# Performance work log

Measured on AMD Instinct MI355X. Metric: run time of the kernel, lower is better.

Reference implementation:

```python
import jax, jax.numpy as jnp
import numpy as np

TOP_K = 2


def setup_inputs() -> dict:
    key = jax.random.key(0)
    k0, k1, k2, k3, k4 = jax.random.split(key, 5)
    B, S, H, F, E = 2, 1024, 2048, 7168, 8
    scale = 0.02
    return {
        "hidden_states": jax.random.normal(k0, (B, S, H), jnp.float32),
        "Wg": jax.random.normal(k1, (E, H), jnp.float32) * scale,
        "w1": jax.random.normal(k2, (E, F, H), jnp.float32) * scale,
        "w3": jax.random.normal(k3, (E, F, H), jnp.float32) * scale,
        "w2": jax.random.normal(k4, (E, H, F), jnp.float32) * scale,
    }


def reference(hidden_states, Wg, w1, w3, w2):
    B, S, H = hidden_states.shape
    E = Wg.shape[0]
    x = hidden_states.reshape(-1, H)                      # [T, H]
    T = x.shape[0]

    # Router: logits -> softmax (float32) -> top-k -> renormalize
    router_logits = jnp.einsum("th,eh->te", x, Wg)        # [T, E]
    probs = jax.nn.softmax(router_logits.astype(jnp.float32), axis=-1)
    top_w, top_idx = jax.lax.top_k(probs, TOP_K)          # [T, K]
    top_w = top_w / jnp.sum(top_w, axis=-1, keepdims=True)
    top_w = top_w.astype(x.dtype)

    # Combine weights: [T, E], zero for unselected experts
    combine = jnp.zeros((T, E), x.dtype).at[
        jnp.arange(T)[:, None], top_idx
    ].add(top_w)

    out = jnp.zeros((T, H), x.dtype)
    for e in range(E):
        h = jax.nn.silu(x @ w1[e].T) * (x @ w3[e].T)      # [T, F]
        out = out + (h @ w2[e].T) * combine[:, e:e + 1]   # [T, H]

    return out.reshape(B, S, H), router_logits
```

## Files before the change

kernel.cpp:

```cpp
#include <hip/hip_runtime.h>

#define T_TOK 2048
#define H_DIM 2048
#define F_DIM 7168
#define E_NUM 8
#define MAX_SLOTS 5120
#define N13 (2 * F_DIM)

typedef __attribute__((ext_vector_type(8))) _Float16 f16x8;
typedef __attribute__((ext_vector_type(4))) float    f32x4;

#define GLL(g, l) __builtin_amdgcn_global_load_lds(                          \
    (const __attribute__((address_space(1))) void*)(g),                      \
    (__attribute__((address_space(3))) void*)(l), 16, 0, 0)


__global__ __launch_bounds__(256) void cvt13_kernel(const float* __restrict__ w1,
                                                    const float* __restrict__ w3,
                                                    _Float16* __restrict__ w13h) {
    int b = blockIdx.x;
    int e = b / N13;
    int c = b - e * N13;
    int blk = c >> 6, sub = c & 63;
    int f = blk * 32 + (sub & 31);
    const float* src = (sub < 32 ? w1 : w3) + ((size_t)e * F_DIM + f) * H_DIM + threadIdx.x * 8;
    _Float16* dst = w13h + (size_t)b * H_DIM + threadIdx.x * 8;
    float4 a = *(const float4*)src;
    float4 bb = *(const float4*)(src + 4);
    f16x8 h;
    h[0]=(_Float16)a.x;  h[1]=(_Float16)a.y;  h[2]=(_Float16)a.z;  h[3]=(_Float16)a.w;
    h[4]=(_Float16)bb.x; h[5]=(_Float16)bb.y; h[6]=(_Float16)bb.z; h[7]=(_Float16)bb.w;
    *(f16x8*)dst = h;
}

__global__ __launch_bounds__(256) void cvtw_kernel(const float* __restrict__ src,
                                                   _Float16* __restrict__ dst) {
    size_t i = ((size_t)blockIdx.x * 256 + threadIdx.x) * 8;
    float4 a = *(const float4*)(src + i);
    float4 b = *(const float4*)(src + i + 4);
    f16x8 h;
    h[0]=(_Float16)a.x; h[1]=(_Float16)a.y; h[2]=(_Float16)a.z; h[3]=(_Float16)a.w;
    h[4]=(_Float16)b.x; h[5]=(_Float16)b.y; h[6]=(_Float16)b.z; h[7]=(_Float16)b.w;
    *(f16x8*)(dst + i) = h;
}


__global__ __launch_bounds__(256) void router_kernel(
    const float* __restrict__ x, const float* __restrict__ wg,
    float* __restrict__ logits_out, int* __restrict__ tk_e,
    float* __restrict__ tk_w, int* __restrict__ meta) {
    int wave = threadIdx.x >> 6;
    int lane = threadIdx.x & 63;
    int t = blockIdx.x * 4 + wave;
    const float* xr = x + (size_t)t * H_DIM;

    float xv[32];
#pragma unroll
    for (int i = 0; i < 8; i++) {
        float4 v = *(const float4*)(xr + i * 256 + lane * 4);
        xv[i*4+0] = v.x; xv[i*4+1] = v.y; xv[i*4+2] = v.z; xv[i*4+3] = v.w;
    }
    float lg[E_NUM];
#pragma unroll
    for (int e = 0; e < E_NUM; e++) {
        const float* wr = wg + (size_t)e * H_DIM;
        float acc = 0.f;
#pragma unroll
        for (int i = 0; i < 8; i++) {
            float4 v = *(const float4*)(wr + i * 256 + lane * 4);
            acc += xv[i*4+0]*v.x + xv[i*4+1]*v.y + xv[i*4+2]*v.z + xv[i*4+3]*v.w;
        }
#pragma unroll
        for (int s = 32; s > 0; s >>= 1) acc += __shfl_xor(acc, s, 64);
        lg[e] = acc;
    }
    if (lane == 0) {
        float b0 = -3e38f, b1 = -3e38f; int i0 = 0, i1 = 0;
#pragma unroll
        for (int e = 0; e < E_NUM; e++) {
            float le = lg[e];
            if (le > b0)      { b1 = b0; i1 = i0; b0 = le; i0 = e; }
            else if (le > b1) { b1 = le; i1 = e; }
        }
        float w0 = 1.f / (1.f + __expf(b1 - b0));
        float w1v = 1.f - w0;
#pragma unroll
        for (int e = 0; e < E_NUM; e++) logits_out[(size_t)t * E_NUM + e] = lg[e];
        tk_e[t*2+0] = i0; tk_w[t*2+0] = w0;
        tk_e[t*2+1] = i1; tk_w[t*2+1] = w1v;
        atomicAdd(&meta[i0], 1);
        atomicAdd(&meta[i1], 1);
    }
}

__global__ void scan_kernel(int* __restrict__ meta, int* __restrict__ slot_tok,
                            float* __restrict__ slot_w) {
    int lane = threadIdx.x;
    int cnts[E_NUM], pads[E_NUM], bases[E_NUM];
    int run = 0;
#pragma unroll
    for (int e = 0; e < E_NUM; e++) {
        cnts[e] = meta[e];
        pads[e] = (cnts[e] + 127) & ~127;
        bases[e] = run;
        run += pads[e];
    }
    if (lane < E_NUM) { meta[8 + lane] = pads[lane]; meta[16 + lane] = bases[lane]; }
    for (int e = 0; e < E_NUM; e++)
        for (int i = cnts[e] + lane; i < pads[e]; i += 64) {
            slot_tok[bases[e] + i] = 0;
            slot_w[bases[e] + i] = 0.f;
        }
}

__global__ __launch_bounds__(256) void assign_kernel(
    const int* __restrict__ tk_e, const float* __restrict__ tk_w,
    int* __restrict__ meta, int* __restrict__ slot_tok, float* __restrict__ slot_w) {
    int t = blockIdx.x * 256 + threadIdx.x;
    if (t >= T_TOK) return;
#pragma unroll
    for (int k = 0; k < 2; k++) {
        int e = tk_e[t*2+k];
        int pos = atomicAdd(&meta[24 + e], 1);
        int s = meta[16 + e] + pos;
        slot_tok[s] = t;
        slot_w[s] = tk_w[t*2+k];
    }
}

__global__ __launch_bounds__(512, 2) void ffn1_kernel(
    const _Float16* __restrict__ xb, const _Float16* __restrict__ w13h,
    const int* __restrict__ slot_tok, const int* __restrict__ meta,
    _Float16* __restrict__ hbuf) {
    int e = blockIdx.z;
    int cntpad = meta[8 + e];
    int mb = blockIdx.y;
    if (mb * 256 >= cntpad) return;
    int base = meta[16 + e];
    int nb = blockIdx.x;

    __shared__ _Float16 sA[2][256][64];
    __shared__ _Float16 sB[2][256][64];

    int tid  = threadIdx.x;
    int lane = tid & 63;
    int wave = tid >> 6;
    int wm = wave >> 2, wn = wave & 3;
    int w8 = wave * 8;

    int lr = lane & 15;
    int sw = lane & 7;
    int sg = lane >> 4;
    int offk0 = lr * 64 + ((sg    ) ^ sw) * 8;
    int offk1 = lr * 64 + ((sg + 4) ^ sw) * 8;

    int rsub = lane >> 3;
    int sl   = (lane & 7) ^ rsub;
    int slot0 = base + mb * 256;

    const _Float16* aG[4];
    const _Float16* bG[4];
#pragma unroll
    for (int q = 0; q < 4; q++) {
        int r = mb * 256 + q * 64 + w8 + rsub;
        int tok = (r < cntpad) ? slot_tok[base + r] : 0;
        aG[q] = xb + (size_t)tok * H_DIM + sl * 8;
        bG[q] = w13h + ((size_t)e * N13 + (size_t)nb * 256 + q * 64 + w8 + rsub) * H_DIM + sl * 8;
    }

    f32x4 zero = {0.f, 0.f, 0.f, 0.f};
    f32x4 acc[8][4];
#pragma unroll
    for (int m = 0; m < 8; m++)
#pragma unroll
        for (int n = 0; n < 4; n++) acc[m][n] = zero;

    const int NT = H_DIM / 64;
#pragma unroll
    for (int q = 0; q < 4; q++) GLL(aG[q] + 0,  &sA[0][q*64 + w8][0]);
#pragma unroll
    for (int q = 0; q < 4; q++) GLL(bG[q] + 0,  &sB[0][q*64 + w8][0]);
#pragma unroll
    for (int q = 0; q < 4; q++) GLL(aG[q] + 64, &sA[1][q*64 + w8][0]);
#pragma unroll
    for (int q = 0; q < 4; q++) GLL(bG[q] + 64, &sB[1][q*64 + w8][0]);

    for (int t = 0; t < NT; ++t) {
        if (t < NT - 1) asm volatile("s_waitcnt vmcnt(8)" ::: "memory");
        else            asm volatile("s_waitcnt vmcnt(0)" ::: "memory");
        __builtin_amdgcn_sched_barrier(0);
        __builtin_amdgcn_s_barrier();
        __builtin_amdgcn_sched_barrier(0);
        int bd = t & 1;
        const _Float16* Ab = &sA[bd][wm * 128][0];
        const _Float16* Bb = &sB[bd][wn * 64][0];
        f16x8 bf[2][4];
#pragma unroll
        for (int n = 0; n < 4; n++) {
            bf[0][n] = *(const f16x8*)(const void*)(Bb + n * 1024 + offk0);
            bf[1][n] = *(const f16x8*)(const void*)(Bb + n * 1024 + offk1);
        }
        __builtin_amdgcn_s_setprio(1);
#pragma unroll
        for (int m = 0; m < 8; m++) {
            f16x8 a0 = *(const f16x8*)(const void*)(Ab + m * 1024 + offk0);
            f16x8 a1 = *(const f16x8*)(const void*)(Ab + m * 1024 + offk1);
#pragma unroll
            for (int n = 0; n < 4; n++) {
                acc[m][n] = __builtin_amdgcn_mfma_f32_16x16x32_f16(a0, bf[0][n], acc[m][n], 0, 0, 0);
                acc[m][n] = __builtin_amdgcn_mfma_f32_16x16x32_f16(a1, bf[1][n], acc[m][n], 0, 0, 0);
            }
        }
        __builtin_amdgcn_s_setprio(0);
        __builtin_amdgcn_sched_barrier(0);
        __builtin_amdgcn_s_barrier();
        __builtin_amdgcn_sched_barrier(0);
        if (t + 2 < NT) {
            int k2 = (t + 2) * 64;
#pragma unroll
            for (int q = 0; q < 4; q++) GLL(aG[q] + k2, &sA[bd][q*64 + w8][0]);
#pragma unroll
            for (int q = 0; q < 4; q++) GLL(bG[q] + k2, &sB[bd][q*64 + w8][0]);
        }
    }

    int row_e0 = mb * 256 + wm * 128;
    int fb = nb * 128 + wn * 32;
#pragma unroll
    for (int m = 0; m < 8; m++) {
#pragma unroll
        for (int j = 0; j < 4; j++) {
            int re = row_e0 + m * 16 + (lane >> 4) * 4 + j;
            if (re < cntpad) {
                size_t srow = (size_t)(base + re) * F_DIM;
#pragma unroll
                for (int n = 0; n < 2; n++) {
                    float a1 = acc[m][n][j], a3 = acc[m][n + 2][j];
                    float hv = a1 * a3 / (1.f + __expf(-a1));
                    hbuf[srow + fb + n * 16 + lr] = (_Float16)hv;
                }
            }
        }
    }
}

__global__ __launch_bounds__(512, 2) void ffn2_kernel(
    const _Float16* __restrict__ hbuf, const _Float16* __restrict__ w2h,
    const int* __restrict__ slot_tok, const float* __restrict__ slot_w,
    const int* __restrict__ meta, float* __restrict__ out) {
    int e = blockIdx.z;
    int cntpad = meta[8 + e];
    int mb = blockIdx.y;
    if (mb * 128 >= cntpad) return;
    int base = meta[16 + e];
    int nb = blockIdx.x;

    __shared__ _Float16 sA[2][128][64];
    __shared__ _Float16 sB[2][256][64];

    int tid  = threadIdx.x;
    int lane = tid & 63;
    int wave = tid >> 6;
    int wm = wave >> 2, wn = wave & 3;
    int w8 = wave * 8;

    int lr = lane & 15;
    int sw = lane & 7;
    int sg = lane >> 4;
    int offk0 = lr * 64 + ((sg    ) ^ sw) * 8;
    int offk1 = lr * 64 + ((sg + 4) ^ sw) * 8;

    int rsub = lane >> 3;
    int sl   = (lane & 7) ^ rsub;
    int slot0 = base + mb * 128;

    const _Float16* aG[2];
    const _Float16* bG[4];
#pragma unroll
    for (int q = 0; q < 2; q++)
        aG[q] = hbuf + (size_t)(slot0 + q * 64 + w8 + rsub) * F_DIM + sl * 8;
#pragma unroll
    for (int q = 0; q < 4; q++)
        bG[q] = w2h + ((size_t)e * H_DIM + (size_t)nb * 256 + q * 64 + w8 + rsub) * F_DIM + sl * 8;

    f32x4 zero = {0.f, 0.f, 0.f, 0.f};
    f32x4 acc[4][4];
#pragma unroll
    for (int m = 0; m < 4; m++)
#pragma unroll
        for (int n = 0; n < 4; n++) acc[m][n] = zero;

    const int NT = F_DIM / 64;
#pragma unroll
    for (int q = 0; q < 2; q++) GLL(aG[q] + 0,  &sA[0][q*64 + w8][0]);
#pragma unroll
    for (int q = 0; q < 4; q++) GLL(bG[q] + 0,  &sB[0][q*64 + w8][0]);
#pragma unroll
    for (int q = 0; q < 2; q++) GLL(aG[q] + 64, &sA[1][q*64 + w8][0]);
#pragma unroll
    for (int q = 0; q < 4; q++) GLL(bG[q] + 64, &sB[1][q*64 + w8][0]);

    for (int t = 0; t < NT; ++t) {
        if (t < NT - 1) asm volatile("s_waitcnt vmcnt(6)" ::: "memory");
        else            asm volatile("s_waitcnt vmcnt(0)" ::: "memory");
        __builtin_amdgcn_sched_barrier(0);
        __builtin_amdgcn_s_barrier();
        __builtin_amdgcn_sched_barrier(0);
        int bd = t & 1;
        const _Float16* Ab = &sA[bd][wm * 64][0];
        const _Float16* Bb = &sB[bd][wn * 64][0];
        f16x8 bf[2][4];
#pragma unroll
        for (int n = 0; n < 4; n++) {
            bf[0][n] = *(const f16x8*)(const void*)(Bb + n * 1024 + offk0);
            bf[1][n] = *(const f16x8*)(const void*)(Bb + n * 1024 + offk1);
        }
        __builtin_amdgcn_s_setprio(1);
#pragma unroll
        for (int m = 0; m < 4; m++) {
            f16x8 a0 = *(const f16x8*)(const void*)(Ab + m * 1024 + offk0);
            f16x8 a1 = *(const f16x8*)(const void*)(Ab + m * 1024 + offk1);
#pragma unroll
            for (int n = 0; n < 4; n++) {
                acc[m][n] = __builtin_amdgcn_mfma_f32_16x16x32_f16(a0, bf[0][n], acc[m][n], 0, 0, 0);
                acc[m][n] = __builtin_amdgcn_mfma_f32_16x16x32_f16(a1, bf[1][n], acc[m][n], 0, 0, 0);
            }
        }
        __builtin_amdgcn_s_setprio(0);
        __builtin_amdgcn_sched_barrier(0);
        __builtin_amdgcn_s_barrier();
        __builtin_amdgcn_sched_barrier(0);
        if (t + 2 < NT) {
            int k2 = (t + 2) * 64;
#pragma unroll
            for (int q = 0; q < 2; q++) GLL(aG[q] + k2, &sA[bd][q*64 + w8][0]);
#pragma unroll
            for (int q = 0; q < 4; q++) GLL(bG[q] + k2, &sB[bd][q*64 + w8][0]);
        }
    }

    int row0 = mb * 128 + wm * 64;
    int col0 = nb * 256 + wn * 64;
#pragma unroll
    for (int m = 0; m < 4; m++) {
        int rb = row0 + m * 16 + (lane >> 4) * 4;
        int toks[4]; float wts[4];
#pragma unroll
        for (int j = 0; j < 4; j++) {
            int s = base + rb + j;
            toks[j] = slot_tok[s];
            wts[j]  = slot_w[s];
        }
#pragma unroll
        for (int n = 0; n < 4; n++) {
            int col = col0 + n * 16 + lr;
            f32x4 v = acc[m][n];
#pragma unroll
            for (int j = 0; j < 4; j++)
                atomicAdd(&out[(size_t)toks[j] * H_DIM + col], v[j] * wts[j]);
        }
    }
}

extern "C" void kernel_launch(void* const* d_in, const int* in_sizes, int n_in,
                              void* d_out, int out_size, void* d_ws, size_t ws_size,
                              hipStream_t stream) {
    const float* x  = (const float*)d_in[0];
    const float* wg = (const float*)d_in[1];
    const float* w1 = (const float*)d_in[2];
    const float* w3 = (const float*)d_in[3];
    const float* w2 = (const float*)d_in[4];
    float* out = (float*)d_out;
    float* logits = out + (size_t)T_TOK * H_DIM;

    const size_t WELEM = (size_t)E_NUM * F_DIM * H_DIM;

    char* ws = (char*)d_ws;
    _Float16* w13h = (_Float16*)ws;
    _Float16* w2h  = w13h + 2 * WELEM;
    _Float16* hbuf = w2h + WELEM;
    _Float16* xb   = hbuf + (size_t)MAX_SLOTS * F_DIM;
    char* p = (char*)(xb + (size_t)T_TOK * H_DIM);
    int*   slot_tok = (int*)p;   p += MAX_SLOTS * 4;
    float* slot_w   = (float*)p; p += MAX_SLOTS * 4;
    int*   tk_e     = (int*)p;   p += T_TOK * 2 * 4;
    float* tk_w     = (float*)p; p += T_TOK * 2 * 4;
    int*   meta     = (int*)p;

    hipMemsetAsync(d_out, 0, (size_t)out_size * sizeof(float), stream);
    hipMemsetAsync(meta, 0, 32 * sizeof(int), stream);

    cvt13_kernel<<<dim3(E_NUM * N13), 256, 0, stream>>>(w1, w3, w13h);
    cvtw_kernel<<<dim3(WELEM / (256 * 8)), 256, 0, stream>>>(w2, w2h);
    cvtw_kernel<<<dim3((size_t)T_TOK * H_DIM / (256 * 8)), 256, 0, stream>>>(x, xb);

    router_kernel<<<dim3(T_TOK / 4), 256, 0, stream>>>(x, wg, logits, tk_e, tk_w, meta);
    scan_kernel<<<dim3(1), 64, 0, stream>>>(meta, slot_tok, slot_w);
    assign_kernel<<<dim3(T_TOK / 256), 256, 0, stream>>>(tk_e, tk_w, meta, slot_tok, slot_w);

    ffn1_kernel<<<dim3(N13 / 256, 8, E_NUM), 512, 0, stream>>>(xb, w13h, slot_tok, meta, hbuf);
    ffn2_kernel<<<dim3(H_DIM / 256, 16, E_NUM), 512, 0, stream>>>(hbuf, w2h, slot_tok, slot_w, meta, out);
}
```

Baseline: 1.292 ms.

## Interleave A-chunk prefetch with MFMA and split-K FFN2 with 256-row tiles

Pads expert slots to 256 so row bounds checks can be dropped. The FFN1 and FFN2 main loops now split the A tile into four 64-row chunks and issue each chunk's global-to-LDS load between MFMA groups, using finer-grained barriers to overlap loads with compute. FFN2 moves to 256x256 tiles with a two-way split over the F dimension (grid z doubled), which relies on the existing atomicAdd output. The trade-off is more padding work, more atomics into the output, and more frequent barriers per K step.

```diff
diff --git a/kernel.cpp b/kernel.cpp
--- a/kernel.cpp
+++ b/kernel.cpp
@@ -4,7 +4,7 @@
 #define H_DIM 2048
 #define F_DIM 7168
 #define E_NUM 8
-#define MAX_SLOTS 5120
+#define MAX_SLOTS 6144
 #define N13 (2 * F_DIM)
 
 typedef __attribute__((ext_vector_type(8))) _Float16 f16x8;
@@ -101,7 +101,7 @@
 #pragma unroll
     for (int e = 0; e < E_NUM; e++) {
         cnts[e] = meta[e];
-        pads[e] = (cnts[e] + 127) & ~127;
+        pads[e] = (cnts[e] + 255) & ~255;
         bases[e] = run;
         run += pads[e];
     }
@@ -127,6 +127,7 @@
         slot_w[s] = tk_w[t*2+k];
     }
 }
+
 
 __global__ __launch_bounds__(512, 2) void ffn1_kernel(
     const _Float16* __restrict__ xb, const _Float16* __restrict__ w13h,
@@ -139,7 +140,7 @@
     int base = meta[16 + e];
     int nb = blockIdx.x;
 
-    __shared__ _Float16 sA[2][256][64];
+    __shared__ _Float16 sA[2][4][64][64];
     __shared__ _Float16 sB[2][256][64];
 
     int tid  = threadIdx.x;
@@ -147,26 +148,26 @@
     int wave = tid >> 6;
     int wm = wave >> 2, wn = wave & 3;
     int w8 = wave * 8;
-
-    int lr = lane & 15;
-    int sw = lane & 7;
-    int sg = lane >> 4;
-    int offk0 = lr * 64 + ((sg    ) ^ sw) * 8;
-    int offk1 = lr * 64 + ((sg + 4) ^ sw) * 8;
+    int lr  = lane & 15;
+    int sg  = lane >> 4;
+    int sw7 = lane & 7;
+    int so0 = ((sg    ) ^ sw7) * 8;
+    int so1 = ((sg + 4) ^ sw7) * 8;
 
     int rsub = lane >> 3;
-    int sl   = (lane & 7) ^ rsub;
-    int slot0 = base + mb * 256;
-
-    const _Float16* aG[4];
-    const _Float16* bG[4];
-#pragma unroll
-    for (int q = 0; q < 4; q++) {
-        int r = mb * 256 + q * 64 + w8 + rsub;
-        int tok = (r < cntpad) ? slot_tok[base + r] : 0;
-        aG[q] = xb + (size_t)tok * H_DIM + sl * 8;
-        bG[q] = w13h + ((size_t)e * N13 + (size_t)nb * 256 + q * 64 + w8 + rsub) * H_DIM + sl * 8;
-    }
+    int sl   = sw7 ^ rsub;
+    int s    = w8 + rsub;
+    const _Float16* aP[4];
+#pragma unroll
+    for (int c = 0; c < 4; c++) {
+        int trow = (s >> 5) * 128 + c * 32 + (s & 31);
+        int tok = slot_tok[base + mb * 256 + trow];
+        aP[c] = xb + (size_t)tok * H_DIM + sl * 8;
+    }
+    const _Float16* bP[4];
+#pragma unroll
+    for (int q = 0; q < 4; q++)
+        bP[q] = w13h + ((size_t)e * N13 + (size_t)nb * 256 + q * 64 + s) * H_DIM + sl * 8;
 
     f32x4 zero = {0.f, 0.f, 0.f, 0.f};
     f32x4 acc[8][4];
@@ -176,69 +177,86 @@
         for (int n = 0; n < 4; n++) acc[m][n] = zero;
 
     const int NT = H_DIM / 64;
-#pragma unroll
-    for (int q = 0; q < 4; q++) GLL(aG[q] + 0,  &sA[0][q*64 + w8][0]);
-#pragma unroll
-    for (int q = 0; q < 4; q++) GLL(bG[q] + 0,  &sB[0][q*64 + w8][0]);
-#pragma unroll
-    for (int q = 0; q < 4; q++) GLL(aG[q] + 64, &sA[1][q*64 + w8][0]);
-#pragma unroll
-    for (int q = 0; q < 4; q++) GLL(bG[q] + 64, &sB[1][q*64 + w8][0]);
+
+#pragma unroll
+    for (int c = 0; c < 4; c++) GLL(aP[c], &sA[0][c][w8][0]);
+#pragma unroll
+    for (int q = 0; q < 4; q++) GLL(bP[q], &sB[0][q * 64 + w8][0]);
+#pragma unroll
+    for (int c = 0; c < 3; c++) GLL(aP[c] + 64, &sA[1][c][w8][0]);
 
     for (int t = 0; t < NT; ++t) {
-        if (t < NT - 1) asm volatile("s_waitcnt vmcnt(8)" ::: "memory");
-        else            asm volatile("s_waitcnt vmcnt(0)" ::: "memory");
+        int cur = t & 1, nxt = cur ^ 1;
+        int kA1 = (t + 1) * 64, kA2 = (t + 2) * 64;
+
+        if (t + 1 < NT) {
+            GLL(aP[3] + kA1, &sA[nxt][3][w8][0]);
+            GLL(bP[0] + kA1, &sB[nxt][       w8][0]);
+            GLL(bP[1] + kA1, &sB[nxt][ 64 + w8][0]);
+            GLL(bP[2] + kA1, &sB[nxt][128 + w8][0]);
+            GLL(bP[3] + kA1, &sB[nxt][192 + w8][0]);
+            asm volatile("s_waitcnt vmcnt(8)" ::: "memory");
+        } else {
+            asm volatile("s_waitcnt vmcnt(0)" ::: "memory");
+        }
         __builtin_amdgcn_sched_barrier(0);
         __builtin_amdgcn_s_barrier();
-        __builtin_amdgcn_sched_barrier(0);
-        int bd = t & 1;
-        const _Float16* Ab = &sA[bd][wm * 128][0];
-        const _Float16* Bb = &sB[bd][wn * 64][0];
-        f16x8 bf[2][4];
+
+        f16x8 bf[4][2];
 #pragma unroll
         for (int n = 0; n < 4; n++) {
-            bf[0][n] = *(const f16x8*)(const void*)(Bb + n * 1024 + offk0);
-            bf[1][n] = *(const f16x8*)(const void*)(Bb + n * 1024 + offk1);
-        }
-        __builtin_amdgcn_s_setprio(1);
-#pragma unroll
-        for (int m = 0; m < 8; m++) {
-            f16x8 a0 = *(const f16x8*)(const void*)(Ab + m * 1024 + offk0);
-            f16x8 a1 = *(const f16x8*)(const void*)(Ab + m * 1024 + offk1);
+            bf[n][0] = *(const f16x8*)(const void*)&sB[cur][wn * 64 + n * 16 + lr][so0];
+            bf[n][1] = *(const f16x8*)(const void*)&sB[cur][wn * 64 + n * 16 + lr][so1];
+        }
+        {
+            f16x8 af0 = *(const f16x8*)(const void*)&sA[cur][0][wm * 32 + lr][so0];
+            f16x8 af1 = *(const f16x8*)(const void*)&sA[cur][0][wm * 32 + lr][so1];
+            f16x8 ag0 = *(const f16x8*)(const void*)&sA[cur][0][wm * 32 + 16 + lr][so0];
+            f16x8 ag1 = *(const f16x8*)(const void*)&sA[cur][0][wm * 32 + 16 + lr][so1];
+            __builtin_amdgcn_s_setprio(1);
 #pragma unroll
             for (int n = 0; n < 4; n++) {
-                acc[m][n] = __builtin_amdgcn_mfma_f32_16x16x32_f16(a0, bf[0][n], acc[m][n], 0, 0, 0);
-                acc[m][n] = __builtin_amdgcn_mfma_f32_16x16x32_f16(a1, bf[1][n], acc[m][n], 0, 0, 0);
+                acc[0][n] = __builtin_amdgcn_mfma_f32_16x16x32_f16(af0, bf[n][0], acc[0][n], 0, 0, 0);
+                acc[0][n] = __builtin_amdgcn_mfma_f32_16x16x32_f16(af1, bf[n][1], acc[0][n], 0, 0, 0);
+                acc[1][n] = __builtin_amdgcn_mfma_f32_16x16x32_f16(ag0, bf[n][0], acc[1][n], 0, 0, 0);
+                acc[1][n] = __builtin_amdgcn_mfma_f32_16x16x32_f16(ag1, bf[n][1], acc[1][n], 0, 0, 0);
             }
-        }
-        __builtin_amdgcn_s_setprio(0);
-        __builtin_amdgcn_sched_barrier(0);
+            __builtin_amdgcn_s_setprio(0);
+        }
         __builtin_amdgcn_s_barrier();
-        __builtin_amdgcn_sched_barrier(0);
-        if (t + 2 < NT) {
-            int k2 = (t + 2) * 64;
-#pragma unroll
-            for (int q = 0; q < 4; q++) GLL(aG[q] + k2, &sA[bd][q*64 + w8][0]);
-#pragma unroll
-            for (int q = 0; q < 4; q++) GLL(bG[q] + k2, &sB[bd][q*64 + w8][0]);
-        }
-    }
-
-    int row_e0 = mb * 256 + wm * 128;
-    int fb = nb * 128 + wn * 32;
+
+#pragma unroll
+        for (int q = 1; q < 4; ++q) {
+            if (t + 2 < NT) GLL(aP[q - 1] + kA2, &sA[cur][q - 1][w8][0]);
+            f16x8 af0 = *(const f16x8*)(const void*)&sA[cur][q][wm * 32 + lr][so0];
+            f16x8 af1 = *(const f16x8*)(const void*)&sA[cur][q][wm * 32 + lr][so1];
+            f16x8 ag0 = *(const f16x8*)(const void*)&sA[cur][q][wm * 32 + 16 + lr][so0];
+            f16x8 ag1 = *(const f16x8*)(const void*)&sA[cur][q][wm * 32 + 16 + lr][so1];
+            __builtin_amdgcn_s_setprio(1);
+#pragma unroll
+            for (int n = 0; n < 4; n++) {
+                acc[q*2+0][n] = __builtin_amdgcn_mfma_f32_16x16x32_f16(af0, bf[n][0], acc[q*2+0][n], 0, 0, 0);
+                acc[q*2+0][n] = __builtin_amdgcn_mfma_f32_16x16x32_f16(af1, bf[n][1], acc[q*2+0][n], 0, 0, 0);
+                acc[q*2+1][n] = __builtin_amdgcn_mfma_f32_16x16x32_f16(ag0, bf[n][0], acc[q*2+1][n], 0, 0, 0);
+                acc[q*2+1][n] = __builtin_amdgcn_mfma_f32_16x16x32_f16(ag1, bf[n][1], acc[q*2+1][n], 0, 0, 0);
+            }
+            __builtin_amdgcn_s_setprio(0);
+            __builtin_amdgcn_s_barrier();
+        }
+    }
+
+    int fb = (nb * 4 + wn) * 32;
 #pragma unroll
     for (int m = 0; m < 8; m++) {
 #pragma unroll
         for (int j = 0; j < 4; j++) {
-            int re = row_e0 + m * 16 + (lane >> 4) * 4 + j;
-            if (re < cntpad) {
-                size_t srow = (size_t)(base + re) * F_DIM;
-#pragma unroll
-                for (int n = 0; n < 2; n++) {
-                    float a1 = acc[m][n][j], a3 = acc[m][n + 2][j];
-                    float hv = a1 * a3 / (1.f + __expf(-a1));
-                    hbuf[srow + fb + n * 16 + lr] = (_Float16)hv;
-                }
+            int re = mb * 256 + wm * 128 + m * 16 + sg * 4 + j;
+            size_t srow = (size_t)(base + re) * F_DIM;
+#pragma unroll
+            for (int p = 0; p < 2; p++) {
+                float a1v = acc[m][p][j], a3v = acc[m][p + 2][j];
+                float hv = a1v * a3v / (1.f + __expf(-a1v));
+                hbuf[srow + fb + p * 16 + lr] = (_Float16)hv;
             }
         }
     }
@@ -248,14 +266,17 @@
     const _Float16* __restrict__ hbuf, const _Float16* __restrict__ w2h,
     const int* __restrict__ slot_tok, const float* __restrict__ slot_w,
     const int* __restrict__ meta, float* __restrict__ out) {
-    int e = blockIdx.z;
+    int ez = blockIdx.z;
+    int e = ez >> 1, ks = ez & 1;
     int cntpad = meta[8 + e];
     int mb = blockIdx.y;
-    if (mb * 128 >= cntpad) return;
+    if (mb * 256 >= cntpad) return;
     int base = meta[16 + e];
     int nb = blockIdx.x;
-
-    __shared__ _Float16 sA[2][128][64];
+    const int KOFF = ks * (F_DIM / 2);
+    const int NT = (F_DIM / 2) / 64;
+
+    __shared__ _Float16 sA[2][4][64][64];
     __shared__ _Float16 sB[2][256][64];
 
     int tid  = threadIdx.x;
@@ -263,93 +284,111 @@
     int wave = tid >> 6;
     int wm = wave >> 2, wn = wave & 3;
     int w8 = wave * 8;
-
-    int lr = lane & 15;
-    int sw = lane & 7;
-    int sg = lane >> 4;
-    int offk0 = lr * 64 + ((sg    ) ^ sw) * 8;
-    int offk1 = lr * 64 + ((sg + 4) ^ sw) * 8;
+    int lr  = lane & 15;
+    int sg  = lane >> 4;
+    int sw7 = lane & 7;
+    int so0 = ((sg    ) ^ sw7) * 8;
+    int so1 = ((sg + 4) ^ sw7) * 8;
 
     int rsub = lane >> 3;
-    int sl   = (lane & 7) ^ rsub;
-    int slot0 = base + mb * 128;
-
-    const _Float16* aG[2];
-    const _Float16* bG[4];
-#pragma unroll
-    for (int q = 0; q < 2; q++)
-        aG[q] = hbuf + (size_t)(slot0 + q * 64 + w8 + rsub) * F_DIM + sl * 8;
+    int sl   = sw7 ^ rsub;
+    int s    = w8 + rsub;
+    const _Float16* aP[4];
+#pragma unroll
+    for (int c = 0; c < 4; c++) {
+        int trow = (s >> 5) * 128 + c * 32 + (s & 31);
+        aP[c] = hbuf + (size_t)(base + mb * 256 + trow) * F_DIM + KOFF + sl * 8;
+    }
+    const _Float16* bP[4];
 #pragma unroll
     for (int q = 0; q < 4; q++)
-        bG[q] = w2h + ((size_t)e * H_DIM + (size_t)nb * 256 + q * 64 + w8 + rsub) * F_DIM + sl * 8;
+        bP[q] = w2h + ((size_t)e * H_DIM + (size_t)nb * 256 + q * 64 + s) * F_DIM + KOFF + sl * 8;
 
     f32x4 zero = {0.f, 0.f, 0.f, 0.f};
-    f32x4 acc[4][4];
-#pragma unroll
-    for (int m = 0; m < 4; m++)
+    f32x4 acc[8][4];
+#pragma unroll
+    for (int m = 0; m < 8; m++)
 #pragma unroll
         for (int n = 0; n < 4; n++) acc[m][n] = zero;
 
-    const int NT = F_DIM / 64;
-#pragma unroll
-    for (int q = 0; q < 2; q++) GLL(aG[q] + 0,  &sA[0][q*64 + w8][0]);
-#pragma unroll
-    for (int q = 0; q < 4; q++) GLL(bG[q] + 0,  &sB[0][q*64 + w8][0]);
-#pragma unroll
-    for (int q = 0; q < 2; q++) GLL(aG[q] + 64, &sA[1][q*64 + w8][0]);
-#pragma unroll
-    for (int q = 0; q < 4; q++) GLL(bG[q] + 64, &sB[1][q*64 + w8][0]);
+#pragma unroll
+    for (int c = 0; c < 4; c++) GLL(aP[c], &sA[0][c][w8][0]);
+#pragma unroll
+    for (int q = 0; q < 4; q++) GLL(bP[q], &sB[0][q * 64 + w8][0]);
+#pragma unroll
+    for (int c = 0; c < 3; c++) GLL(aP[c] + 64, &sA[1][c][w8][0]);
 
     for (int t = 0; t < NT; ++t) {
-        if (t < NT - 1) asm volatile("s_waitcnt vmcnt(6)" ::: "memory");
-        else            asm volatile("s_waitcnt vmcnt(0)" ::: "memory");
+        int cur = t & 1, nxt = cur ^ 1;
+        int kA1 = (t + 1) * 64, kA2 = (t + 2) * 64;
+
+        if (t + 1 < NT) {
+            GLL(aP[3] + kA1, &sA[nxt][3][w8][0]);
+            GLL(bP[0] + kA1, &sB[nxt][       w8][0]);
+            GLL(bP[1] + kA1, &sB[nxt][ 64 + w8][0]);
+            GLL(bP[2] + kA1, &sB[nxt][128 + w8][0]);
+            GLL(bP[3] + kA1, &sB[nxt][192 + w8][0]);
+            asm volatile("s_waitcnt vmcnt(8)" ::: "memory");
+        } else {
+            asm volatile("s_waitcnt vmcnt(0)" ::: "memory");
+        }
         __builtin_amdgcn_sched_barrier(0);
         __builtin_amdgcn_s_barrier();
-        __builtin_amdgcn_sched_barrier(0);
-        int bd = t & 1;
-        const _Float16* Ab = &sA[bd][wm * 64][0];
-        const _Float16* Bb = &sB[bd][wn * 64][0];
-        f16x8 bf[2][4];
+
+        f16x8 bf[4][2];
 #pragma unroll
         for (int n = 0; n < 4; n++) {
-            bf[0][n] = *(const f16x8*)(const void*)(Bb + n * 1024 + offk0);
-            bf[1][n] = *(const f16x8*)(const void*)(Bb + n * 1024 + offk1);
-        }
-        __builtin_amdgcn_s_setprio(1);
-#pragma unroll
-        for (int m = 0; m < 4; m++) {
-            f16x8 a0 = *(const f16x8*)(const void*)(Ab + m * 1024 + offk0);
-            f16x8 a1 = *(const f16x8*)(const void*)(Ab + m * 1024 + offk1);
+            bf[n][0] = *(const f16x8*)(const void*)&sB[cur][wn * 64 + n * 16 + lr][so0];
+            bf[n][1] = *(const f16x8*)(const void*)&sB[cur][wn * 64 + n * 16 + lr][so1];
+        }
+        {
+            f16x8 af0 = *(const f16x8*)(const void*)&sA[cur][0][wm * 32 + lr][so0];
+            f16x8 af1 = *(const f16x8*)(const void*)&sA[cur][0][wm * 32 + lr][so1];
+            f16x8 ag0 = *(const f16x8*)(const void*)&sA[cur][0][wm * 32 + 16 + lr][so0];
+            f16x8 ag1 = *(const f16x8*)(const void*)&sA[cur][0][wm * 32 + 16 + lr][so1];
+            __builtin_amdgcn_s_setprio(1);
 #pragma unroll
             for (int n = 0; n < 4; n++) {
-                acc[m][n] = __builtin_amdgcn_mfma_f32_16x16x32_f16(a0, bf[0][n], acc[m][n], 0, 0, 0);
-                acc[m][n] = __builtin_amdgcn_mfma_f32_16x16x32_f16(a1, bf[1][n], acc[m][n], 0, 0, 0);
+                acc[0][n] = __builtin_amdgcn_mfma_f32_16x16x32_f16(af0, bf[n][0], acc[0][n], 0, 0, 0);
+                acc[0][n] = __builtin_amdgcn_mfma_f32_16x16x32_f16(af1, bf[n][1], acc[0][n], 0, 0, 0);
+                acc[1][n] = __builtin_amdgcn_mfma_f32_16x16x32_f16(ag0, bf[n][0], acc[1][n], 0, 0, 0);
+                acc[1][n] = __builtin_amdgcn_mfma_f32_16x16x32_f16(ag1, bf[n][1], acc[1][n], 0, 0, 0);
             }
-        }
-        __builtin_amdgcn_s_setprio(0);
-        __builtin_amdgcn_sched_barrier(0);
+            __builtin_amdgcn_s_setprio(0);
+        }
         __builtin_amdgcn_s_barrier();
-        __builtin_amdgcn_sched_barrier(0);
-        if (t + 2 < NT) {
-            int k2 = (t + 2) * 64;
-#pragma unroll
-            for (int q = 0; q < 2; q++) GLL(aG[q] + k2, &sA[bd][q*64 + w8][0]);
-#pragma unroll
-            for (int q = 0; q < 4; q++) GLL(bG[q] + k2, &sB[bd][q*64 + w8][0]);
-        }
-    }
-
-    int row0 = mb * 128 + wm * 64;
+
+#pragma unroll
+        for (int q = 1; q < 4; ++q) {
+            if (t + 2 < NT) GLL(aP[q - 1] + kA2, &sA[cur][q - 1][w8][0]);
+            f16x8 af0 = *(const f16x8*)(const void*)&sA[cur][q][wm * 32 + lr][so0];
+            f16x8 af1 = *(const f16x8*)(const void*)&sA[cur][q][wm * 32 + lr][so1];
+            f16x8 ag0 = *(const f16x8*)(const void*)&sA[cur][q][wm * 32 + 16 + lr][so0];
+            f16x8 ag1 = *(const f16x8*)(const void*)&sA[cur][q][wm * 32 + 16 + lr][so1];
+            __builtin_amdgcn_s_setprio(1);
+#pragma unroll
+            for (int n = 0; n < 4; n++) {
+                acc[q*2+0][n] = __builtin_amdgcn_mfma_f32_16x16x32_f16(af0, bf[n][0], acc[q*2+0][n], 0, 0, 0);
+                acc[q*2+0][n] = __builtin_amdgcn_mfma_f32_16x16x32_f16(af1, bf[n][1], acc[q*2+0][n], 0, 0, 0);
+                acc[q*2+1][n] = __builtin_amdgcn_mfma_f32_16x16x32_f16(ag0, bf[n][0], acc[q*2+1][n], 0, 0, 0);
+                acc[q*2+1][n] = __builtin_amdgcn_mfma_f32_16x16x32_f16(ag1, bf[n][1], acc[q*2+1][n], 0, 0, 0);
+            }
+            __builtin_amdgcn_s_setprio(0);
+            __builtin_amdgcn_s_barrier();
+        }
+    }
+
+    int row0 = mb * 256 + wm * 128;
     int col0 = nb * 256 + wn * 64;
 #pragma unroll
-    for (int m = 0; m < 4; m++) {
-        int rb = row0 + m * 16 + (lane >> 4) * 4;
+    for (int m = 0; m < 8; m++) {
+        int rbw = row0 + m * 16 + sg * 4;
         int toks[4]; float wts[4];
 #pragma unroll
         for (int j = 0; j < 4; j++) {
-            int s = base + rb + j;
-            toks[j] = slot_tok[s];
-            wts[j]  = slot_w[s];
+            int sdx = base + rbw + j;
+            toks[j] = slot_tok[sdx];
+            wts[j]  = slot_w[sdx];
         }
 #pragma unroll
         for (int n = 0; n < 4; n++) {
@@ -398,6 +437,6 @@
     scan_kernel<<<dim3(1), 64, 0, stream>>>(meta, slot_tok, slot_w);
     assign_kernel<<<dim3(T_TOK / 256), 256, 0, stream>>>(tk_e, tk_w, meta, slot_tok, slot_w);
 
-    ffn1_kernel<<<dim3(N13 / 256, 8, E_NUM), 512, 0, stream>>>(xb, w13h, slot_tok, meta, hbuf);
-    ffn2_kernel<<<dim3(H_DIM / 256, 16, E_NUM), 512, 0, stream>>>(hbuf, w2h, slot_tok, slot_w, meta, out);
-}
+    ffn1_kernel<<<dim3(N13 / 256, 16, E_NUM), 512, 0, stream>>>(xb, w13h, slot_tok, meta, hbuf);
+    ffn2_kernel<<<dim3(H_DIM / 256, 16, E_NUM * 2), 512, 0, stream>>>(hbuf, w2h, slot_tok, slot_w, meta, out);
+}
```

After: 1.533 ms. 18.7% more time.
